# Performance work log

Measured on AMD Instinct MI355X. Metric: run time of the kernel, lower is better.

## Reference

```python
import jax, jax.numpy as jnp
import numpy as np

B, N, D, P, V = 8, 256, 300, 128, 50001  # batch, seq len, emb dim, proj dim, vocab(+unk)


def setup_inputs() -> dict:
    key = jax.random.key(0)
    ks = jax.random.split(key, 10)
    s = 1.0 / np.sqrt(D)
    sp = 1.0 / np.sqrt(P)
    emb = jax.random.normal(ks[0], (V, D), jnp.float32)
    emb = emb.at[-1].set(0.0)  # unk row zeroed, matches add_unk
    return {
        "sentence": jax.random.randint(ks[1], (B, N), 0, V),
        "emb": emb,
        "Wl": jax.random.uniform(ks[2], (P, D), jnp.float32, -s, s),
        "bl": jnp.zeros((P,), jnp.float32),
        "Wr": jax.random.uniform(ks[3], (P, D), jnp.float32, -s, s),
        "Wo": jax.random.uniform(ks[4], (1, P), jnp.float32, -sp, sp),
        "bo": jnp.zeros((1,), jnp.float32),
        "Ws1": jax.random.uniform(ks[5], (P, D), jnp.float32, -s, s),
        "bs1": jnp.zeros((P,), jnp.float32),
        "Ws2": jax.random.uniform(ks[6], (1, P), jnp.float32, -sp, sp),
        "bs2": jnp.zeros((1,), jnp.float32),
        "We1": jax.random.uniform(ks[7], (P, D), jnp.float32, -s, s),
        "be1": jnp.zeros((P,), jnp.float32),
        "We2": jax.random.uniform(ks[8], (1, P), jnp.float32, -sp, sp),
        "be2": jnp.zeros((1,), jnp.float32),
    }


def reference(sentence, emb, Wl, bl, Wr, Wo, bo, Ws1, bs1, Ws2, bs2, We1, be1, We2, be2):
    x = emb[sentence]                                   # [B,N,D] embedding lookup
    start = jax.nn.relu(x @ Ws1.T + bs1) @ Ws2.T + bs2  # [B,N,1]
    end = jax.nn.relu(x @ We1.T + be1) @ We2.T + be2    # [B,N,1]
    left = x @ Wl.T + bl                                # [B,N,P]
    right = x @ Wr.T                                    # [B,N,P]
    # proj[b,i,j,p] = left[b,j,p] + right[b,i,p]  (unsqueeze(1) + unsqueeze(2))
    proj = left[:, None, :, :] + right[:, :, None, :]   # [B,N,N,P]
    bigram = jax.nn.relu(proj) @ Wo.T + bo              # [B,N,N,1]
    return (bigram, start, end)
```

## Files before the change

### kernel.cpp

```cpp
#include <hip/hip_runtime.h>

#define NB 8
#define NN 256
#define DD 300
#define PP 128
#define NC 512
#define OFF_S (NB * NN * NN)
#define OFF_E (NB * NN * NN + NB * NN)

typedef unsigned short u16;
typedef unsigned int   u32;

__device__ __forceinline__ float bf2f(u16 u) {
    union { u32 i; float f; } v;
    v.i = ((u32)u) << 16;
    return v.f;
}
__device__ __forceinline__ u16 f2bf(float f) {
    union { float f; u32 i; } v;
    v.f = f;
    u32 lsb = (v.i >> 16) & 1u;
    v.i += 0x7fffu + lsb;
    return (u16)(v.i >> 16);
}

template<bool BF>
__device__ __forceinline__ float4 ld4(const void* base, int idx) {
    if (BF) {
        ushort4 e = *(const ushort4*)((const u16*)base + idx);
        return make_float4(bf2f(e.x), bf2f(e.y), bf2f(e.z), bf2f(e.w));
    } else {
        return *(const float4*)((const float*)base + idx);
    }
}
template<bool BF>
__device__ __forceinline__ float ld1(const void* base, int idx) {
    return BF ? bf2f(((const u16*)base)[idx]) : ((const float*)base)[idx];
}
template<bool BF>
__device__ __forceinline__ void st1(void* base, int idx, float v) {
    if (BF) ((u16*)base)[idx] = f2bf(v);
    else    ((float*)base)[idx] = v;
}
template<bool BF>
__device__ __forceinline__ void st4(void* base, int idx, float4 v) {
    if (BF) {
        ushort4 o = make_ushort4(f2bf(v.x), f2bf(v.y), f2bf(v.z), f2bf(v.w));
        *(ushort4*)((u16*)base + idx) = o;
    } else {
        *(float4*)((float*)base + idx) = v;
    }
}
__device__ __forceinline__ float4 rfma4(float4 l, float r, float w, float4 a) {
    a.x = fmaf(fmaxf(l.x + r, 0.f), w, a.x);
    a.y = fmaf(fmaxf(l.y + r, 0.f), w, a.y);
    a.z = fmaf(fmaxf(l.z + r, 0.f), w, a.z);
    a.w = fmaf(fmaxf(l.w + r, 0.f), w, a.w);
    return a;
}

__device__ __forceinline__ int flag_wave(const u32* __restrict__ embU) {
    int lane = threadIdx.x & 63;
    int cnt = 0;
    for (int i = lane; i < 256; i += 64) {
        u32 w = embU[i];
        union { u32 u; float f; } v;
        v.u = (w & 0xFFFFu) << 16;
        float a = fabsf(v.f);
        if (a == 0.f || (a >= 0.00390625f && a <= 256.f)) cnt++;
    }
    #pragma unroll
    for (int off = 32; off; off >>= 1) cnt += __shfl_xor(cnt, off, 64);
    return (cnt >= 128) ? 1 : 0;
}

template<bool BF>
__device__ __forceinline__ void prep_body(
    const void* __restrict__ Wl, const void* __restrict__ Wr,
    const void* __restrict__ Ws1, const void* __restrict__ We1,
    float* __restrict__ WTf, float (*tile)[301])
{
    const int tid = threadIdx.x;
    const int c0  = blockIdx.x * 32;

    for (int e = tid; e < 32 * 75; e += 256) {
        int r = e / 75;
        int q = e - r * 75;
        int c = c0 + r;
        const void* src = (c < 128) ? Wl : (c < 256) ? Wr
                        : (c < 384) ? Ws1 : We1;
        float4 f = ld4<BF>(src, (c & 127) * DD + 4 * q);
        tile[r][4 * q + 0] = f.x;
        tile[r][4 * q + 1] = f.y;
        tile[r][4 * q + 2] = f.z;
        tile[r][4 * q + 3] = f.w;
    }
    __syncthreads();
    for (int e = tid; e < 300 * 32; e += 256) {
        int k = e >> 5;
        int c = e & 31;
        WTf[(size_t)k * NC + c0 + c] = tile[c][k];
    }
}

extern "C" __global__ void __launch_bounds__(256)
prep_kernel(const void* __restrict__ Wl, const void* __restrict__ Wr,
            const void* __restrict__ Ws1, const void* __restrict__ We1,
            float* __restrict__ WTf, const u32* __restrict__ embU)
{
    __shared__ float tile[32][301];
    __shared__ int sflag;
    if (threadIdx.x < 64) {
        int f = flag_wave(embU);
        if (threadIdx.x == 0) sflag = f;
    }
    __syncthreads();
    if (sflag) prep_body<true >(Wl, Wr, Ws1, We1, WTf, tile);
    else       prep_body<false>(Wl, Wr, Ws1, We1, WTf, tile);
}

template<bool BF>
__device__ __forceinline__ void tok_body(
    const int* __restrict__ sent, const void* __restrict__ emb,
    const float* __restrict__ WTf,
    const void* __restrict__ bl,
    const void* __restrict__ bs1, const void* __restrict__ Ws2,
    const void* __restrict__ bs2,
    const void* __restrict__ be1, const void* __restrict__ We2,
    const void* __restrict__ be2,
    float* __restrict__ leftT, float* __restrict__ rightW,
    void* __restrict__ out, float (*sxT)[8], int* sids)
{
    const int tid = threadIdx.x;
    const int t0  = blockIdx.x * 8;

    if (tid < 8) sids[tid] = sent[t0 + tid];
    __syncthreads();

    for (int e = tid; e < DD * 8; e += 256) {
        int k = e >> 3, t = e & 7;
        sxT[k][t] = ld1<BF>(emb, sids[t] * DD + k);
    }
    __syncthreads();

    float a0[8], a1[8];
    #pragma unroll
    for (int t = 0; t < 8; ++t) { a0[t] = 0.f; a1[t] = 0.f; }

    const float* wp = WTf + 2 * tid;
#define LW(kk) (*(const float2*)(wp + (size_t)(kk) * NC))
#define FMAK(kk, Wv) do {                                               \
        float4 xa = *(const float4*)&sxT[(kk)][0];                      \
        float4 xb = *(const float4*)&sxT[(kk)][4];                      \
        float wx_ = (Wv).x, wy_ = (Wv).y;                               \
        a0[0]=fmaf(xa.x,wx_,a0[0]); a1[0]=fmaf(xa.x,wy_,a1[0]);         \
        a0[1]=fmaf(xa.y,wx_,a0[1]); a1[1]=fmaf(xa.y,wy_,a1[1]);         \
        a0[2]=fmaf(xa.z,wx_,a0[2]); a1[2]=fmaf(xa.z,wy_,a1[2]);         \
        a0[3]=fmaf(xa.w,wx_,a0[3]); a1[3]=fmaf(xa.w,wy_,a1[3]);         \
        a0[4]=fmaf(xb.x,wx_,a0[4]); a1[4]=fmaf(xb.x,wy_,a1[4]);         \
        a0[5]=fmaf(xb.y,wx_,a0[5]); a1[5]=fmaf(xb.y,wy_,a1[5]);         \
        a0[6]=fmaf(xb.z,wx_,a0[6]); a1[6]=fmaf(xb.z,wy_,a1[6]);         \
        a0[7]=fmaf(xb.w,wx_,a0[7]); a1[7]=fmaf(xb.w,wy_,a1[7]);         \
    } while (0)

    float2 q0 = LW(0), q1 = LW(1), q2 = LW(2),
           q3 = LW(3), q4 = LW(4), q5 = LW(5);
    for (int k = 0; k < DD; k += 6) {
        float2 u0 = q0, u1 = q1, u2 = q2, u3 = q3, u4 = q4, u5 = q5;
        if (k + 6 < DD) {
            q0 = LW(k + 6);  q1 = LW(k + 7);  q2 = LW(k + 8);
            q3 = LW(k + 9);  q4 = LW(k + 10); q5 = LW(k + 11);
        }
        FMAK(k + 0, u0); FMAK(k + 1, u1); FMAK(k + 2, u2);
        FMAK(k + 3, u3); FMAK(k + 4, u4); FMAK(k + 5, u5);
    }
#undef LW
#undef FMAK

    const int wv = tid >> 6;
    const int l  = tid & 63;
    const int p0 = 2 * l, p1 = p0 + 1;

    if (wv == 0) {
        float b0 = ld1<BF>(bl, p0), b1 = ld1<BF>(bl, p1);
        const int bb = t0 >> 8, j0 = t0 & 255;
        float* o0 = leftT + ((size_t)bb * PP + p0) * NN + j0;
        float* o1 = leftT + ((size_t)bb * PP + p1) * NN + j0;
        #pragma unroll
        for (int t = 0; t < 8; ++t) { o0[t] = a0[t] + b0; o1[t] = a1[t] + b1; }
    } else if (wv == 1) {
        #pragma unroll
        for (int t = 0; t < 8; ++t) {
            rightW[(size_t)(t0 + t) * PP + p0] = a0[t];
            rightW[(size_t)(t0 + t) * PP + p1] = a1[t];
        }
    } else {
        const void* h1 = (wv == 2) ? bs1 : be1;
        const void* h2 = (wv == 2) ? Ws2 : We2;
        const void* h3 = (wv == 2) ? bs2 : be2;
        float b0 = ld1<BF>(h1, p0), b1 = ld1<BF>(h1, p1);
        float w0h = ld1<BF>(h2, p0), w1h = ld1<BF>(h2, p1);
        float v[8];
        #pragma unroll
        for (int t = 0; t < 8; ++t)
            v[t] = fmaxf(a0[t] + b0, 0.f) * w0h + fmaxf(a1[t] + b1, 0.f) * w1h;
        #pragma unroll
        for (int off = 32; off; off >>= 1) {
            #pragma unroll
            for (int t = 0; t < 8; ++t) v[t] += __shfl_down(v[t], off, 64);
        }
        if (l == 0) {
            float b2 = ld1<BF>(h3, 0);
            int base = (wv == 2) ? OFF_S : OFF_E;
            #pragma unroll
            for (int t = 0; t < 8; ++t)
                st1<BF>(out, base + t0 + t, v[t] + b2);
        }
    }
}

extern "C" __global__ void __launch_bounds__(256)
tok_kernel(const int* __restrict__ sent, const void* __restrict__ emb,
           const float* __restrict__ WTf,
           const void* __restrict__ bl,
           const void* __restrict__ bs1, const void* __restrict__ Ws2,
           const void* __restrict__ bs2,
           const void* __restrict__ be1, const void* __restrict__ We2,
           const void* __restrict__ be2,
           float* __restrict__ leftT, float* __restrict__ rightW,
           void* __restrict__ out)
{
    __shared__ __align__(16) float sxT[DD][8];
    __shared__ int sids[8];
    __shared__ int sflag;
    if (threadIdx.x < 64) {
        int f = flag_wave((const u32*)emb);
        if (threadIdx.x == 0) sflag = f;
    }
    if (threadIdx.x < 8) sids[threadIdx.x] = sent[blockIdx.x * 8 + threadIdx.x];
    __syncthreads();
    if (sflag) {
        tok_body<true >(sent, emb, WTf, bl, bs1, Ws2, bs2, be1, We2, be2,
                        leftT, rightW, out, sxT, sids);
    } else {
        tok_body<false>(sent, emb, WTf, bl, bs1, Ws2, bs2, be1, We2, be2,
                        leftT, rightW, out, sxT, sids);
    }
}

template<bool BF>
__device__ __forceinline__ void big_body(
    const float* __restrict__ leftT, const float* __restrict__ rightW,
    const void* __restrict__ Wo, const void* __restrict__ bo,
    void* __restrict__ outB,
    float (*sR)[128], float* sWo, float4 (*red4)[64][4])
{
    const int tid = threadIdx.x;
    const int b   = blockIdx.x >> 6;
    const int i0  = (blockIdx.x & 63) << 2;

    if (tid < 128) sWo[tid] = ld1<BF>(Wo, tid);
    for (int c = tid; c < 512; c += 256) {
        int i = c >> 7, pp = c & 127;
        sR[i][pp] = rightW[((size_t)(b * NN + i0 + i)) * PP + pp];
    }
    __syncthreads();

    const int w    = tid >> 6;
    const int lane = tid & 63;
    const int j4   = lane << 2;
    const float* lp = leftT + (size_t)b * PP * NN + j4;

    float4 A0 = {0.f, 0.f, 0.f, 0.f}, A1 = A0, A2 = A0, A3 = A0;
    const int pbase = w * 32;
    #pragma unroll
    for (int g = 0; g < 8; ++g) {
        const int p = pbase + g * 4;
        float4 wo = *(const float4*)&sWo[p];
        float4 r0 = *(const float4*)&sR[0][p];
        float4 r1 = *(const float4*)&sR[1][p];
        float4 r2 = *(const float4*)&sR[2][p];
        float4 r3 = *(const float4*)&sR[3][p];
        const float* lpp = lp + (size_t)p * NN;
        float4 l0 = *(const float4*)(lpp);
        float4 l1 = *(const float4*)(lpp + NN);
        float4 l2 = *(const float4*)(lpp + 2 * NN);
        float4 l3 = *(const float4*)(lpp + 3 * NN);
        A0 = rfma4(l0, r0.x, wo.x, A0);
        A1 = rfma4(l0, r1.x, wo.x, A1);
        A2 = rfma4(l0, r2.x, wo.x, A2);
        A3 = rfma4(l0, r3.x, wo.x, A3);
        A0 = rfma4(l1, r0.y, wo.y, A0);
        A1 = rfma4(l1, r1.y, wo.y, A1);
        A2 = rfma4(l1, r2.y, wo.y, A2);
        A3 = rfma4(l1, r3.y, wo.y, A3);
        A0 = rfma4(l2, r0.z, wo.z, A0);
        A1 = rfma4(l2, r1.z, wo.z, A1);
        A2 = rfma4(l2, r2.z, wo.z, A2);
        A3 = rfma4(l2, r3.z, wo.z, A3);
        A0 = rfma4(l3, r0.w, wo.w, A0);
        A1 = rfma4(l3, r1.w, wo.w, A1);
        A2 = rfma4(l3, r2.w, wo.w, A2);
        A3 = rfma4(l3, r3.w, wo.w, A3);
    }

    red4[w][lane][0] = A0;
    red4[w][lane][1] = A1;
    red4[w][lane][2] = A2;
    red4[w][lane][3] = A3;
    __syncthreads();

    if (tid < 64) {
        float bov = ld1<BF>(bo, 0);
        #pragma unroll
        for (int i = 0; i < 4; ++i) {
            float4 s0 = red4[0][tid][i];
            float4 s1 = red4[1][tid][i];
            float4 s2 = red4[2][tid][i];
            float4 s3 = red4[3][tid][i];
            float4 s;
            s.x = s0.x + s1.x + s2.x + s3.x + bov;
            s.y = s0.y + s1.y + s2.y + s3.y + bov;
            s.z = s0.z + s1.z + s2.z + s3.z + bov;
            s.w = s0.w + s1.w + s2.w + s3.w + bov;
            st4<BF>(outB, (int)(((size_t)(b * NN + i0 + i)) * NN) + tid * 4, s);
        }
    }
}

extern "C" __global__ void __launch_bounds__(256)
big_kernel(const float* __restrict__ leftT, const float* __restrict__ rightW,
           const void* __restrict__ Wo, const void* __restrict__ bo,
           void* __restrict__ outB, const u32* __restrict__ embU)
{
    __shared__ float sR[4][128];
    __shared__ float sWo[128];
    __shared__ float4 red4[4][64][4];
    __shared__ int sflag;
    if (threadIdx.x < 64) {
        int f = flag_wave(embU);
        if (threadIdx.x == 0) sflag = f;
    }
    __syncthreads();
    if (sflag) big_body<true >(leftT, rightW, Wo, bo, outB, sR, sWo, red4);
    else       big_body<false>(leftT, rightW, Wo, bo, outB, sR, sWo, red4);
}

extern "C" void kernel_launch(void* const* d_in, const int* in_sizes, int n_in,
                              void* d_out, int out_size, void* d_ws, size_t ws_size,
                              hipStream_t stream) {
    const int*  sent = (const int*)d_in[0];
    const void* emb  = d_in[1];
    const void* Wl   = d_in[2];
    const void* bl   = d_in[3];
    const void* Wr   = d_in[4];
    const void* Wo   = d_in[5];
    const void* bo   = d_in[6];
    const void* Ws1  = d_in[7];
    const void* bs1  = d_in[8];
    const void* Ws2  = d_in[9];
    const void* bs2  = d_in[10];
    const void* We1  = d_in[11];
    const void* be1  = d_in[12];
    const void* We2  = d_in[13];
    const void* be2  = d_in[14];

    float* leftT  = (float*)((char*)d_ws + 1024);
    float* rightW = leftT + (size_t)NB * PP * NN;
    float* WTf    = rightW + (size_t)NB * NN * PP;

    hipLaunchKernelGGL(prep_kernel, dim3(16), dim3(256), 0, stream,
                       Wl, Wr, Ws1, We1, WTf, (const u32*)emb);
    hipLaunchKernelGGL(tok_kernel, dim3(256), dim3(256), 0, stream,
                       sent, emb, WTf, bl, bs1, Ws2, bs2, be1, We2, be2,
                       leftT, rightW, d_out);
    hipLaunchKernelGGL(big_kernel, dim3(512), dim3(256), 0, stream,
                       leftT, rightW, Wo, bo, d_out, (const u32*)emb);
}
```

Measured before the change: 155.2 us.

## Drop weight-transpose prep kernel; read row-major weights directly in token kernel

Removes the separate prep kernel that transposed Wl/Wr/Ws1/We1 into a packed fp32 buffer. Each wave of the token kernel now streams its own weight matrix row-major with 16-byte vector loads, converting from bf16 when the input is bf16. The goal is to save one kernel launch and the extra global write and read of the transposed weights. Output stores to leftT and rightW are also vectorized. In exchange, per-lane row-strided loads are less coalesced than the old transposed layout.

```diff
diff --git a/kernel.cpp b/kernel.cpp
--- a/kernel.cpp
+++ b/kernel.cpp
@@ -4,7 +4,6 @@
 #define NN 256
 #define DD 300
 #define PP 128
-#define NC 512
 #define OFF_S (NB * NN * NN)
 #define OFF_E (NB * NN * NN + NB * NN)
 
@@ -25,15 +24,6 @@
 }
 
 template<bool BF>
-__device__ __forceinline__ float4 ld4(const void* base, int idx) {
-    if (BF) {
-        ushort4 e = *(const ushort4*)((const u16*)base + idx);
-        return make_float4(bf2f(e.x), bf2f(e.y), bf2f(e.z), bf2f(e.w));
-    } else {
-        return *(const float4*)((const float*)base + idx);
-    }
-}
-template<bool BF>
 __device__ __forceinline__ float ld1(const void* base, int idx) {
     return BF ? bf2f(((const u16*)base)[idx]) : ((const float*)base)[idx];
 }
@@ -58,6 +48,24 @@
     a.w = fmaf(fmaxf(l.w + r, 0.f), w, a.w);
     return a;
 }
+
+template<bool BF> struct wraw;
+template<> struct wraw<false> {
+    typedef float4 T;
+    static __device__ __forceinline__ T ld(const void* W, int off) {
+        return *(const float4*)((const float*)W + off);
+    }
+    static __device__ __forceinline__ float4 cvt(T v) { return v; }
+};
+template<> struct wraw<true> {
+    typedef ushort4 T;
+    static __device__ __forceinline__ T ld(const void* W, int off) {
+        return *(const ushort4*)((const u16*)W + off);
+    }
+    static __device__ __forceinline__ float4 cvt(T v) {
+        return make_float4(bf2f(v.x), bf2f(v.y), bf2f(v.z), bf2f(v.w));
+    }
+};
 
 __device__ __forceinline__ int flag_wave(const u32* __restrict__ embU) {
     int lane = threadIdx.x & 63;
@@ -75,84 +83,40 @@
 }
 
 template<bool BF>
-__device__ __forceinline__ void prep_body(
-    const void* __restrict__ Wl, const void* __restrict__ Wr,
+__device__ __forceinline__ void tok_body(
+    const void* __restrict__ Wl,  const void* __restrict__ Wr,
     const void* __restrict__ Ws1, const void* __restrict__ We1,
-    float* __restrict__ WTf, float (*tile)[301])
-{
-    const int tid = threadIdx.x;
-    const int c0  = blockIdx.x * 32;
-
-    for (int e = tid; e < 32 * 75; e += 256) {
-        int r = e / 75;
-        int q = e - r * 75;
-        int c = c0 + r;
-        const void* src = (c < 128) ? Wl : (c < 256) ? Wr
-                        : (c < 384) ? Ws1 : We1;
-        float4 f = ld4<BF>(src, (c & 127) * DD + 4 * q);
-        tile[r][4 * q + 0] = f.x;
-        tile[r][4 * q + 1] = f.y;
-        tile[r][4 * q + 2] = f.z;
-        tile[r][4 * q + 3] = f.w;
-    }
-    __syncthreads();
-    for (int e = tid; e < 300 * 32; e += 256) {
-        int k = e >> 5;
-        int c = e & 31;
-        WTf[(size_t)k * NC + c0 + c] = tile[c][k];
-    }
-}
-
-extern "C" __global__ void __launch_bounds__(256)
-prep_kernel(const void* __restrict__ Wl, const void* __restrict__ Wr,
-            const void* __restrict__ Ws1, const void* __restrict__ We1,
-            float* __restrict__ WTf, const u32* __restrict__ embU)
-{
-    __shared__ float tile[32][301];
-    __shared__ int sflag;
-    if (threadIdx.x < 64) {
-        int f = flag_wave(embU);
-        if (threadIdx.x == 0) sflag = f;
-    }
-    __syncthreads();
-    if (sflag) prep_body<true >(Wl, Wr, Ws1, We1, WTf, tile);
-    else       prep_body<false>(Wl, Wr, Ws1, We1, WTf, tile);
-}
-
-template<bool BF>
-__device__ __forceinline__ void tok_body(
-    const int* __restrict__ sent, const void* __restrict__ emb,
-    const float* __restrict__ WTf,
     const void* __restrict__ bl,
     const void* __restrict__ bs1, const void* __restrict__ Ws2,
     const void* __restrict__ bs2,
     const void* __restrict__ be1, const void* __restrict__ We2,
     const void* __restrict__ be2,
+    const void* __restrict__ emb,
     float* __restrict__ leftT, float* __restrict__ rightW,
-    void* __restrict__ out, float (*sxT)[8], int* sids)
+    void* __restrict__ out, float (*sxT)[8], const int* sids)
 {
     const int tid = threadIdx.x;
     const int t0  = blockIdx.x * 8;
 
-    if (tid < 8) sids[tid] = sent[t0 + tid];
-    __syncthreads();
-
     for (int e = tid; e < DD * 8; e += 256) {
         int k = e >> 3, t = e & 7;
         sxT[k][t] = ld1<BF>(emb, sids[t] * DD + k);
     }
     __syncthreads();
 
+    const int wv = tid >> 6;
+    const int l  = tid & 63;
+    const int p0 = 2 * l, p1 = p0 + 1;
+    const void* Wm = (wv == 0) ? Wl : (wv == 1) ? Wr : (wv == 2) ? Ws1 : We1;
+    const int r0 = p0 * DD, r1 = p1 * DD;
+
     float a0[8], a1[8];
     #pragma unroll
     for (int t = 0; t < 8; ++t) { a0[t] = 0.f; a1[t] = 0.f; }
 
-    const float* wp = WTf + 2 * tid;
-#define LW(kk) (*(const float2*)(wp + (size_t)(kk) * NC))
-#define FMAK(kk, Wv) do {                                               \
+#define FMAK(kk, wx_, wy_) do {                                         \
         float4 xa = *(const float4*)&sxT[(kk)][0];                      \
         float4 xb = *(const float4*)&sxT[(kk)][4];                      \
-        float wx_ = (Wv).x, wy_ = (Wv).y;                               \
         a0[0]=fmaf(xa.x,wx_,a0[0]); a1[0]=fmaf(xa.x,wy_,a1[0]);         \
         a0[1]=fmaf(xa.y,wx_,a0[1]); a1[1]=fmaf(xa.y,wy_,a1[1]);         \
         a0[2]=fmaf(xa.z,wx_,a0[2]); a1[2]=fmaf(xa.z,wy_,a1[2]);         \
@@ -163,36 +127,48 @@
         a0[7]=fmaf(xb.w,wx_,a0[7]); a1[7]=fmaf(xb.w,wy_,a1[7]);         \
     } while (0)
 
-    float2 q0 = LW(0), q1 = LW(1), q2 = LW(2),
-           q3 = LW(3), q4 = LW(4), q5 = LW(5);
-    for (int k = 0; k < DD; k += 6) {
-        float2 u0 = q0, u1 = q1, u2 = q2, u3 = q3, u4 = q4, u5 = q5;
-        if (k + 6 < DD) {
-            q0 = LW(k + 6);  q1 = LW(k + 7);  q2 = LW(k + 8);
-            q3 = LW(k + 9);  q4 = LW(k + 10); q5 = LW(k + 11);
-        }
-        FMAK(k + 0, u0); FMAK(k + 1, u1); FMAK(k + 2, u2);
-        FMAK(k + 3, u3); FMAK(k + 4, u4); FMAK(k + 5, u5);
-    }
-#undef LW
+#define GROUP(k0, U0, U1) do {                                          \
+        float4 f0_ = wraw<BF>::cvt(U0);                                 \
+        float4 f1_ = wraw<BF>::cvt(U1);                                 \
+        FMAK((k0) + 0, f0_.x, f1_.x);                                   \
+        FMAK((k0) + 1, f0_.y, f1_.y);                                   \
+        FMAK((k0) + 2, f0_.z, f1_.z);                                   \
+        FMAK((k0) + 3, f0_.w, f1_.w);                                   \
+    } while (0)
+
+    typedef typename wraw<BF>::T WT;
+    WT w0a = wraw<BF>::ld(Wm, r0 + 0), w1a = wraw<BF>::ld(Wm, r1 + 0);
+    WT w0b = wraw<BF>::ld(Wm, r0 + 4), w1b = wraw<BF>::ld(Wm, r1 + 4);
+    WT w0c = wraw<BF>::ld(Wm, r0 + 8), w1c = wraw<BF>::ld(Wm, r1 + 8);
+    for (int it = 0; it < 25; ++it) {
+        WT u0a = w0a, u1a = w1a, u0b = w0b, u1b = w1b, u0c = w0c, u1c = w1c;
+        const int kn = it * 12 + 12;
+        if (it < 24) {
+            w0a = wraw<BF>::ld(Wm, r0 + kn);     w1a = wraw<BF>::ld(Wm, r1 + kn);
+            w0b = wraw<BF>::ld(Wm, r0 + kn + 4); w1b = wraw<BF>::ld(Wm, r1 + kn + 4);
+            w0c = wraw<BF>::ld(Wm, r0 + kn + 8); w1c = wraw<BF>::ld(Wm, r1 + kn + 8);
+        }
+        GROUP(it * 12,     u0a, u1a);
+        GROUP(it * 12 + 4, u0b, u1b);
+        GROUP(it * 12 + 8, u0c, u1c);
+    }
+#undef GROUP
 #undef FMAK
-
-    const int wv = tid >> 6;
-    const int l  = tid & 63;
-    const int p0 = 2 * l, p1 = p0 + 1;
 
     if (wv == 0) {
         float b0 = ld1<BF>(bl, p0), b1 = ld1<BF>(bl, p1);
         const int bb = t0 >> 8, j0 = t0 & 255;
         float* o0 = leftT + ((size_t)bb * PP + p0) * NN + j0;
         float* o1 = leftT + ((size_t)bb * PP + p1) * NN + j0;
-        #pragma unroll
-        for (int t = 0; t < 8; ++t) { o0[t] = a0[t] + b0; o1[t] = a1[t] + b1; }
+        *(float4*)(o0)     = make_float4(a0[0]+b0, a0[1]+b0, a0[2]+b0, a0[3]+b0);
+        *(float4*)(o0 + 4) = make_float4(a0[4]+b0, a0[5]+b0, a0[6]+b0, a0[7]+b0);
+        *(float4*)(o1)     = make_float4(a1[0]+b1, a1[1]+b1, a1[2]+b1, a1[3]+b1);
+        *(float4*)(o1 + 4) = make_float4(a1[4]+b1, a1[5]+b1, a1[6]+b1, a1[7]+b1);
     } else if (wv == 1) {
         #pragma unroll
         for (int t = 0; t < 8; ++t) {
-            rightW[(size_t)(t0 + t) * PP + p0] = a0[t];
-            rightW[(size_t)(t0 + t) * PP + p1] = a1[t];
+            *(float2*)&rightW[(size_t)(t0 + t) * PP + p0] =
+                make_float2(a0[t], a1[t]);
         }
     } else {
         const void* h1 = (wv == 2) ? bs1 : be1;
@@ -221,7 +197,8 @@
 
 extern "C" __global__ void __launch_bounds__(256)
 tok_kernel(const int* __restrict__ sent, const void* __restrict__ emb,
-           const float* __restrict__ WTf,
+           const void* __restrict__ Wl,  const void* __restrict__ Wr,
+           const void* __restrict__ Ws1, const void* __restrict__ We1,
            const void* __restrict__ bl,
            const void* __restrict__ bs1, const void* __restrict__ Ws2,
            const void* __restrict__ bs2,
@@ -240,11 +217,11 @@
     if (threadIdx.x < 8) sids[threadIdx.x] = sent[blockIdx.x * 8 + threadIdx.x];
     __syncthreads();
     if (sflag) {
-        tok_body<true >(sent, emb, WTf, bl, bs1, Ws2, bs2, be1, We2, be2,
-                        leftT, rightW, out, sxT, sids);
+        tok_body<true >(Wl, Wr, Ws1, We1, bl, bs1, Ws2, bs2, be1, We2, be2,
+                        emb, leftT, rightW, out, sxT, sids);
     } else {
-        tok_body<false>(sent, emb, WTf, bl, bs1, Ws2, bs2, be1, We2, be2,
-                        leftT, rightW, out, sxT, sids);
+        tok_body<false>(Wl, Wr, Ws1, We1, bl, bs1, Ws2, bs2, be1, We2, be2,
+                        emb, leftT, rightW, out, sxT, sids);
     }
 }
 
@@ -367,13 +344,10 @@
 
     float* leftT  = (float*)((char*)d_ws + 1024);
     float* rightW = leftT + (size_t)NB * PP * NN;
-    float* WTf    = rightW + (size_t)NB * NN * PP;
-
-    hipLaunchKernelGGL(prep_kernel, dim3(16), dim3(256), 0, stream,
-                       Wl, Wr, Ws1, We1, WTf, (const u32*)emb);
+
     hipLaunchKernelGGL(tok_kernel, dim3(256), dim3(256), 0, stream,
-                       sent, emb, WTf, bl, bs1, Ws2, bs2, be1, We2, be2,
-                       leftT, rightW, d_out);
+                       sent, emb, Wl, Wr, Ws1, We1, bl, bs1, Ws2, bs2,
+                       be1, We2, be2, leftT, rightW, d_out);
     hipLaunchKernelGGL(big_kernel, dim3(512), dim3(256), 0, stream,
                        leftT, rightW, Wo, bo, d_out, (const u32*)emb);
 }
```

New measurement: 148.0 us. 1.05x faster.
